# Kernel optimization log

Hardware: AMD Instinct MI355X
Metric: run time of the kernel (lower is better)

Reference implementation:

```python
import jax, jax.numpy as jnp
import numpy as np

L = 16            # number_of_grid_levels
T = 524288        # max_hash_table_entries (2^19)
F = 2             # hash_table_feature_dim
MIN_RES = 16      # coarsest_resolution
MAX_RES = 2048    # finest_resolution
WIDTH = 64        # mlp_width
OUT = 3           # output_channels
N = 1048576       # number of 2D query points
PRIME_Y = np.uint32(2654435761)  # NGP spatial hash prime for dim 1 (dim 0 prime = 1)


def _resolutions():
    g = np.exp((np.log(MAX_RES) - np.log(MIN_RES)) / (L - 1))
    return np.floor(MIN_RES * g ** np.arange(L)).astype(np.float32)  # [L]


def setup_inputs() -> dict:
    key = jax.random.key(0)
    ks = jax.random.split(key, 6)
    x = jax.random.uniform(ks[0], (N, 2), dtype=jnp.float32)
    # NGP hash tables are initialized small uniform
    tables = jax.random.uniform(ks[1], (L, T, F), minval=-1e-4, maxval=1e-4, dtype=jnp.float32)
    def dense(k, fi, fo):
        return (jax.random.normal(k, (fi, fo), dtype=jnp.float32) / np.sqrt(fi).astype(np.float32))
    W0 = dense(ks[2], L * F, WIDTH)
    W1 = dense(ks[3], WIDTH, WIDTH)
    W2 = dense(ks[4], WIDTH, OUT)
    return dict(x=x, tables=tables,
                W0=W0, b0=jnp.zeros((WIDTH,), jnp.float32),
                W1=W1, b1=jnp.zeros((WIDTH,), jnp.float32),
                W2=W2, b2=jnp.zeros((OUT,), jnp.float32))


def _hash_encode(x, tables):
    # Multi-resolution hash grid encoding (Instant-NGP, spatial_dim=2).
    res = jnp.asarray(_resolutions())                  # [L]
    scaled = x[:, None, :] * res[None, :, None]        # [N, L, 2]
    floored = jnp.floor(scaled)
    frac = scaled - floored                            # [N, L, 2]
    corners = jnp.array([[0, 0], [1, 0], [0, 1], [1, 1]], dtype=jnp.int32)  # [4, 2]
    vert = floored.astype(jnp.int32)[:, :, None, :] + corners[None, None]   # [N, L, 4, 2]
    vu = vert.astype(jnp.uint32)
    h = vu[..., 0] ^ (vu[..., 1] * PRIME_Y)            # spatial hash (prime for dim0 is 1)
    idx = (h % jnp.uint32(T)).astype(jnp.int32)        # [N, L, 4]
    feats = tables[jnp.arange(L)[None, :, None], idx]  # [N, L, 4, F] gather per level
    # bilinear weights: prod over dims of frac (if corner==1) else 1-frac
    wd = jnp.where(corners[None, None] == 1, frac[:, :, None, :], 1.0 - frac[:, :, None, :])
    w = wd[..., 0] * wd[..., 1]                        # [N, L, 4]
    interp = jnp.einsum('nlc,nlcf->nlf', w, feats)     # [N, L, F]
    return interp.reshape(x.shape[0], L * F)           # [N, L*F]


def reference(x, tables, W0, b0, W1, b1, W2, b2):
    h = _hash_encode(x, tables)
    h = jax.nn.relu(h @ W0 + b0)
    h = jax.nn.relu(h @ W1 + b1)
    return jax.nn.sigmoid(h @ W2 + b2)   # [N, 3]
```

## Files before the change

### kernel.cpp

```cpp
#include <hip/hip_runtime.h>

#define LVLS  16
#define TSZ   524288u
#define TMASK (TSZ - 1u)
#define PRIME 2654435761u

__constant__ float RES[LVLS] = {16.f, 22.f, 30.f, 42.f, 58.f, 80.f, 111.f, 153.f,
                                212.f, 294.f, 406.f, 561.f, 776.f, 1072.f, 1482.f, 2048.f};

typedef __bf16 bf16x8 __attribute__((ext_vector_type(8)));
typedef float  f32x4  __attribute__((ext_vector_type(4)));

union Frag {
    uint4          q;
    unsigned       u[4];
    unsigned short s[8];
    bf16x8         v;
};

static __device__ __forceinline__ unsigned short f2bf(float f) {
    unsigned u = __float_as_uint(f);
    u += 0x7FFFu + ((u >> 16) & 1u);
    return (unsigned short)(u >> 16);
}
static __device__ __forceinline__ unsigned pack2(float a, float b) {
    return (unsigned)f2bf(a) | ((unsigned)f2bf(b) << 16);
}
static __device__ __forceinline__ void lds_fence() {
    asm volatile("s_waitcnt lgkmcnt(0)" ::: "memory");
}

static __device__ __forceinline__ unsigned encode_level(
    const float2 xy, const float res, const float* __restrict__ tbf)
{
    const float sx = xy.x * res, sy = xy.y * res;
    const float fx = floorf(sx),  fy = floorf(sy);
    const float ux = sx - fx,     uy = sy - fy;
    const unsigned ix = (unsigned)(int)fx, iy = (unsigned)(int)fy;
    const unsigned hy0 = iy * PRIME, hy1 = (iy + 1u) * PRIME;
    const unsigned i00 = (ix ^ hy0) & TMASK;
    const unsigned i01 = (ix ^ hy1) & TMASK;
    float2 f00, f10, f01, f11;
    if (!(ix & 1u)) {
        const f32x4 a = *(const f32x4*)(tbf + 2u * (i00 & ~1u));
        const f32x4 b = *(const f32x4*)(tbf + 2u * (i01 & ~1u));
        const bool s0 = (i00 & 1u) != 0u;
        const bool s1 = (i01 & 1u) != 0u;
        f00 = s0 ? make_float2(a[2], a[3]) : make_float2(a[0], a[1]);
        f10 = s0 ? make_float2(a[0], a[1]) : make_float2(a[2], a[3]);
        f01 = s1 ? make_float2(b[2], b[3]) : make_float2(b[0], b[1]);
        f11 = s1 ? make_float2(b[0], b[1]) : make_float2(b[2], b[3]);
    } else {
        const unsigned i10 = ((ix + 1u) ^ hy0) & TMASK;
        const unsigned i11 = ((ix + 1u) ^ hy1) & TMASK;
        const float2* tb2 = (const float2*)tbf;
        f00 = tb2[i00]; f10 = tb2[i10];
        f01 = tb2[i01]; f11 = tb2[i11];
    }
    const float w00 = (1.f - ux) * (1.f - uy);
    const float w10 = ux * (1.f - uy);
    const float w01 = (1.f - ux) * uy;
    const float w11 = ux * uy;
    const float e0 = w00*f00.x + w10*f10.x + w01*f01.x + w11*f11.x;
    const float e1 = w00*f00.y + w10*f10.y + w01*f01.y + w11*f11.y;
    return pack2(e0, e1);
}

#define DENSE_TOTAL 3628

__global__ __launch_bounds__(256) void ngp_dehash(
    const float* __restrict__ tables, float2* __restrict__ dense)
{
    const int e = blockIdx.x * 256 + (int)threadIdx.x;
    if (e >= DENSE_TOTAL) return;
    int l, base;
    if      (e >= 1779) { l = 3; base = 1779; }
    else if (e >=  818) { l = 2; base =  818; }
    else if (e >=  289) { l = 1; base =  289; }
    else                { l = 0; base =    0; }
    const int Wd = (l == 0) ? 17 : (l == 1) ? 23 : (l == 2) ? 31 : 43;
    const int r  = e - base;
    const unsigned iy = (unsigned)(r / Wd), ix = (unsigned)(r % Wd);
    const unsigned h = (ix ^ (iy * PRIME)) & TMASK;
    dense[e] = ((const float2*)(tables + (size_t)l * (TSZ * 2u)))[h];
}

__global__ __launch_bounds__(256) void ngp_encode_fine(
    const float* __restrict__ x, const float* __restrict__ tables,
    unsigned* __restrict__ feat, int N)
{
    const int g = blockIdx.x;
    const int r = g & 7;
    const int l = 8 + r;
    const int n = (g >> 3) * 256 + (int)threadIdx.x;
    if (n >= N) return;
    const float2 xy = ((const float2*)x)[n];
    const float* tbf = tables + (size_t)l * (TSZ * 2u);
    feat[(size_t)r * N + n] = encode_level(xy, RES[l], tbf);
}

#define CLVL 8
#define SFEAT_BYTES (8 * CLVL * 64 * 4)
#define SB0_BYTES   (4 * 64 * 16)
#define SB1_BYTES   (8 * 64 * 16)
#define SDENSE_BYTES (DENSE_TOTAL * 8)
#define REGION_BYTES (SB0_BYTES + SB1_BYTES + SDENSE_BYTES)

__global__ __launch_bounds__(512, 4) void ngp_fused(
    const float* __restrict__ x, const float* __restrict__ tables,
    const float2* __restrict__ dense_g,
    const unsigned* __restrict__ feat,
    const float* __restrict__ W0, const float* __restrict__ b0,
    const float* __restrict__ W1, const float* __restrict__ b1,
    const float* __restrict__ W2, const float* __restrict__ b2,
    float* __restrict__ out, int N)
{
    __shared__ __align__(16) unsigned char smem[SFEAT_BYTES + REGION_BYTES];
    unsigned* sfeat = (unsigned*)smem;
    uint4*    sB0   = (uint4*)(smem + SFEAT_BYTES);
    uint4*    sB1   = (uint4*)(smem + SFEAT_BYTES + SB0_BYTES);
    float2*   sdense = (float2*)(smem + SFEAT_BYTES + SB0_BYTES + SB1_BYTES);
    unsigned short (*hscr)[16][72] =
        (unsigned short (*)[16][72])(smem + SFEAT_BYTES);

    const int tid  = threadIdx.x;
    const int lane = tid & 63;
    const int w    = tid >> 6;
    const int c    = lane & 15;
    const int quad = lane >> 4;

    {
        const int f = w;
        if (f < 4) {
            Frag t0;
            #pragma unroll
            for (int j = 0; j < 8; ++j)
                t0.s[j] = f2bf(W0[(quad * 8 + j) * 64 + f * 16 + c]);
            sB0[f * 64 + lane] = t0.q;
        }
        {
            const int kt = f >> 2, tt = f & 3;
            Frag t1;
            #pragma unroll
            for (int j = 0; j < 8; ++j)
                t1.s[j] = f2bf(W1[(kt * 32 + quad * 8 + j) * 64 + tt * 16 + c]);
            sB1[f * 64 + lane] = t1.q;
        }
        for (int e = tid; e < DENSE_TOTAL; e += 512)
            sdense[e] = dense_g[e];
    }
    __syncthreads();

    const int n = blockIdx.x * 512 + tid;
    if (n < N) {
        const float2 xy = ((const float2*)x)[n];
        #pragma unroll
        for (int l = 0; l < 4; ++l) {
            const int off = (l == 0) ? 0 : (l == 1) ? 289 : (l == 2) ? 818 : 1779;
            const int Wd  = (l == 0) ? 17 : (l == 1) ? 23 : (l == 2) ? 31 : 43;
            const float res = RES[l];
            const float sx = xy.x * res, sy = xy.y * res;
            const float fx = floorf(sx),  fy = floorf(sy);
            const float ux = sx - fx,     uy = sy - fy;
            const int ix = (int)fx, iy = (int)fy;
            const int b = off + iy * Wd + ix;
            const float2 f00 = sdense[b],      f10 = sdense[b + 1];
            const float2 f01 = sdense[b + Wd], f11 = sdense[b + Wd + 1];
            const float w00 = (1.f - ux) * (1.f - uy);
            const float w10 = ux * (1.f - uy);
            const float w01 = (1.f - ux) * uy;
            const float w11 = ux * uy;
            const float e0 = w00*f00.x + w10*f10.x + w01*f01.x + w11*f11.x;
            const float e1 = w00*f00.y + w10*f10.y + w01*f01.y + w11*f11.y;
            sfeat[(w * CLVL + l) * 64 + (lane ^ (((l >> 2) & 1) << 4))] = pack2(e0, e1);
        }
        #pragma unroll 2
        for (int l = 4; l < CLVL; ++l) {
            const float* tbf = tables + (size_t)l * (TSZ * 2u);
            const unsigned p = encode_level(xy, RES[l], tbf);
            sfeat[(w * CLVL + l) * 64 + (lane ^ (((l >> 2) & 1) << 4))] = p;
        }
    }
    __syncthreads();

    Frag B0f[4], B1f[8], B2f[2];
    #pragma unroll
    for (int t = 0; t < 4; ++t) B0f[t].q = sB0[t * 64 + lane];
    #pragma unroll
    for (int f = 0; f < 8; ++f) B1f[f].q = sB1[f * 64 + lane];
    #pragma unroll
    for (int f = 0; f < 2; ++f) {
        #pragma unroll
        for (int j = 0; j < 8; ++j) {
            const float v = (c < 3) ? W2[(f * 32 + quad * 8 + j) * 3 + c] : 0.f;
            B2f[f].s[j] = f2bf(v);
        }
    }

    float bias0[4], bias1[4];
    #pragma unroll
    for (int t = 0; t < 4; ++t) { bias0[t] = b0[t * 16 + c]; bias1[t] = b1[t * 16 + c]; }
    const float bias2 = (c < 3) ? b2[c] : 0.f;

    __syncthreads();

    #pragma unroll 1
    for (int it = 0; it < 4; ++it) {
        const int n0 = blockIdx.x * 512 + w * 64 + it * 16;

        Frag a0;
        if (quad < 2) {
            #pragma unroll
            for (int i = 0; i < 4; ++i)
                a0.u[i] = sfeat[(w * CLVL + quad * 4 + i) * 64 + ((it * 16 + c) ^ (quad << 4))];
        } else {
            #pragma unroll
            for (int i = 0; i < 4; ++i)
                a0.u[i] = feat[(size_t)((quad - 2) * 4 + i) * N + n0 + c];
        }

        f32x4 acc0[4];
        #pragma unroll
        for (int t = 0; t < 4; ++t) {
            f32x4 cin = {bias0[t], bias0[t], bias0[t], bias0[t]};
            acc0[t] = __builtin_amdgcn_mfma_f32_16x16x32_bf16(a0.v, B0f[t].v, cin, 0, 0, 0);
        }

        lds_fence();
        #pragma unroll
        for (int t = 0; t < 4; ++t)
            #pragma unroll
            for (int rr = 0; rr < 4; ++rr)
                hscr[w][quad * 4 + rr][t * 16 + c] = f2bf(fmaxf(acc0[t][rr], 0.f));

        lds_fence();
        Frag a1[2];
        #pragma unroll
        for (int kt = 0; kt < 2; ++kt)
            a1[kt].q = *(const uint4*)&hscr[w][c][kt * 32 + quad * 8];

        f32x4 acc1[4];
        #pragma unroll
        for (int t = 0; t < 4; ++t) {
            f32x4 cin = {bias1[t], bias1[t], bias1[t], bias1[t]};
            cin = __builtin_amdgcn_mfma_f32_16x16x32_bf16(a1[0].v, B1f[t].v, cin, 0, 0, 0);
            acc1[t] = __builtin_amdgcn_mfma_f32_16x16x32_bf16(a1[1].v, B1f[4 + t].v, cin, 0, 0, 0);
        }

        lds_fence();
        #pragma unroll
        for (int t = 0; t < 4; ++t)
            #pragma unroll
            for (int rr = 0; rr < 4; ++rr)
                hscr[w][quad * 4 + rr][t * 16 + c] = f2bf(fmaxf(acc1[t][rr], 0.f));

        lds_fence();
        Frag a2[2];
        #pragma unroll
        for (int kt = 0; kt < 2; ++kt)
            a2[kt].q = *(const uint4*)&hscr[w][c][kt * 32 + quad * 8];

        f32x4 cin2 = {bias2, bias2, bias2, bias2};
        cin2 = __builtin_amdgcn_mfma_f32_16x16x32_bf16(a2[0].v, B2f[0].v, cin2, 0, 0, 0);
        f32x4 acc2 = __builtin_amdgcn_mfma_f32_16x16x32_bf16(a2[1].v, B2f[1].v, cin2, 0, 0, 0);

        if (c < 3) {
            #pragma unroll
            for (int rr = 0; rr < 4; ++rr) {
                if (n0 + quad * 4 + rr < N) {
                    const float s = 1.f / (1.f + __expf(-acc2[rr]));
                    out[(size_t)(n0 + quad * 4 + rr) * 3 + c] = s;
                }
            }
        }
    }
}

extern "C" void kernel_launch(void* const* d_in, const int* in_sizes, int n_in,
                              void* d_out, int out_size, void* d_ws, size_t ws_size,
                              hipStream_t stream) {
    const float* x      = (const float*)d_in[0];
    const float* tables = (const float*)d_in[1];
    const float* W0     = (const float*)d_in[2];
    const float* b0     = (const float*)d_in[3];
    const float* W1     = (const float*)d_in[4];
    const float* b1     = (const float*)d_in[5];
    const float* W2     = (const float*)d_in[6];
    const float* b2     = (const float*)d_in[7];
    float* out = (float*)d_out;
    (void)ws_size; (void)n_in; (void)out_size;

    const int N  = in_sizes[0] / 2;
    unsigned* feat  = (unsigned*)d_ws;
    float2*   dense = (float2*)((char*)d_ws + (size_t)8 * N * 4);

    const int FB = (N + 255) / 256;
    const int PB = (N + 511) / 512;
    ngp_dehash<<<(DENSE_TOTAL + 255) / 256, 256, 0, stream>>>(tables, dense);
    ngp_encode_fine<<<8 * FB, 256, 0, stream>>>(x, tables, feat, N);
    ngp_fused<<<PB, 512, 0, stream>>>(x, tables, dense, feat,
                                      W0, b0, W1, b1, W2, b2, out, N);
}
```

Before: 260.5 us.

## Precompute dense corner-pair tables for mid levels and process two points per fine-encode thread

Adds a kernel that de-hashes levels 4-7 into dense tables where each entry holds the x-adjacent corner pair. The fused kernel then needs two 16-byte loads per level instead of four scattered hash-table gathers. The fine-level encoder now handles two points per thread to raise memory-level parallelism. The cost is an extra small launch and about 0.7 MB of workspace.

```diff
diff --git a/kernel.cpp b/kernel.cpp
--- a/kernel.cpp
+++ b/kernel.cpp
@@ -7,6 +7,10 @@
 
 __constant__ float RES[LVLS] = {16.f, 22.f, 30.f, 42.f, 58.f, 80.f, 111.f, 153.f,
                                 212.f, 294.f, 406.f, 561.f, 776.f, 1072.f, 1482.f, 2048.f};
+
+__constant__ int PRES[4] = {58, 80, 111, 153};
+__constant__ int POFF[4] = {0, 3422, 9902, 22334};
+#define PAIR_TOTAL 45896
 
 typedef __bf16 bf16x8 __attribute__((ext_vector_type(8)));
 typedef float  f32x4  __attribute__((ext_vector_type(4)));
@@ -85,6 +89,23 @@
     dense[e] = ((const float2*)(tables + (size_t)l * (TSZ * 2u)))[h];
 }
 
+__global__ __launch_bounds__(256) void ngp_dehash_pair(
+    const float* __restrict__ tables, f32x4* __restrict__ pairs)
+{
+    const int li = blockIdx.y;
+    const int res = PRES[li];
+    const int cnt = (res + 1) * res;
+    const int e = blockIdx.x * 256 + (int)threadIdx.x;
+    if (e >= cnt) return;
+    const unsigned iy = (unsigned)(e / res), ix = (unsigned)(e % res);
+    const unsigned hy = iy * PRIME;
+    const float2* tb2 = (const float2*)(tables + (size_t)(4 + li) * (TSZ * 2u));
+    const float2 v0 = tb2[(ix ^ hy) & TMASK];
+    const float2 v1 = tb2[((ix + 1u) ^ hy) & TMASK];
+    f32x4 p; p[0] = v0.x; p[1] = v0.y; p[2] = v1.x; p[3] = v1.y;
+    pairs[POFF[li] + e] = p;
+}
+
 __global__ __launch_bounds__(256) void ngp_encode_fine(
     const float* __restrict__ x, const float* __restrict__ tables,
     unsigned* __restrict__ feat, int N)
@@ -92,11 +113,18 @@
     const int g = blockIdx.x;
     const int r = g & 7;
     const int l = 8 + r;
-    const int n = (g >> 3) * 256 + (int)threadIdx.x;
-    if (n >= N) return;
-    const float2 xy = ((const float2*)x)[n];
+    const int n0 = (g >> 3) * 512 + (int)threadIdx.x;
+    const int n1 = n0 + 256;
     const float* tbf = tables + (size_t)l * (TSZ * 2u);
-    feat[(size_t)r * N + n] = encode_level(xy, RES[l], tbf);
+    const float res = RES[l];
+    float2 xy0, xy1;
+    if (n0 < N) xy0 = ((const float2*)x)[n0];
+    if (n1 < N) xy1 = ((const float2*)x)[n1];
+    unsigned p0 = 0, p1 = 0;
+    if (n0 < N) p0 = encode_level(xy0, res, tbf);
+    if (n1 < N) p1 = encode_level(xy1, res, tbf);
+    if (n0 < N) feat[(size_t)r * N + n0] = p0;
+    if (n1 < N) feat[(size_t)r * N + n1] = p1;
 }
 
 #define CLVL 8
@@ -107,8 +135,9 @@
 #define REGION_BYTES (SB0_BYTES + SB1_BYTES + SDENSE_BYTES)
 
 __global__ __launch_bounds__(512, 4) void ngp_fused(
-    const float* __restrict__ x, const float* __restrict__ tables,
+    const float* __restrict__ x,
     const float2* __restrict__ dense_g,
+    const f32x4* __restrict__ pairs,
     const unsigned* __restrict__ feat,
     const float* __restrict__ W0, const float* __restrict__ b0,
     const float* __restrict__ W1, const float* __restrict__ b1,
@@ -174,11 +203,25 @@
             const float e1 = w00*f00.y + w10*f10.y + w01*f01.y + w11*f11.y;
             sfeat[(w * CLVL + l) * 64 + (lane ^ (((l >> 2) & 1) << 4))] = pack2(e0, e1);
         }
-        #pragma unroll 2
-        for (int l = 4; l < CLVL; ++l) {
-            const float* tbf = tables + (size_t)l * (TSZ * 2u);
-            const unsigned p = encode_level(xy, RES[l], tbf);
-            sfeat[(w * CLVL + l) * 64 + (lane ^ (((l >> 2) & 1) << 4))] = p;
+        #pragma unroll
+        for (int li = 0; li < 4; ++li) {
+            const int l = 4 + li;
+            const float res = RES[l];
+            const int Wp = PRES[li];
+            const float sx = xy.x * res, sy = xy.y * res;
+            const float fx = floorf(sx),  fy = floorf(sy);
+            const float ux = sx - fx,     uy = sy - fy;
+            const int ix = (int)fx, iy = (int)fy;
+            const int b = POFF[li] + iy * Wp + ix;
+            const f32x4 r0 = pairs[b];
+            const f32x4 r1 = pairs[b + Wp];
+            const float w00 = (1.f - ux) * (1.f - uy);
+            const float w10 = ux * (1.f - uy);
+            const float w01 = (1.f - ux) * uy;
+            const float w11 = ux * uy;
+            const float e0 = w00*r0[0] + w10*r0[2] + w01*r1[0] + w11*r1[2];
+            const float e1 = w00*r0[1] + w10*r0[3] + w01*r1[1] + w11*r1[3];
+            sfeat[(w * CLVL + l) * 64 + (lane ^ (((l >> 2) & 1) << 4))] = pack2(e0, e1);
         }
     }
     __syncthreads();
@@ -293,11 +336,16 @@
     const int N  = in_sizes[0] / 2;
     unsigned* feat  = (unsigned*)d_ws;
     float2*   dense = (float2*)((char*)d_ws + (size_t)8 * N * 4);
-
-    const int FB = (N + 255) / 256;
+    f32x4*    pairs = (f32x4*)((char*)d_ws + (size_t)8 * N * 4 + DENSE_TOTAL * 8);
+
+    const int FB = (N + 511) / 512;
     const int PB = (N + 511) / 512;
     ngp_dehash<<<(DENSE_TOTAL + 255) / 256, 256, 0, stream>>>(tables, dense);
+    {
+        dim3 g((153 * 154 + 255) / 256, 4);
+        ngp_dehash_pair<<<g, 256, 0, stream>>>(tables, pairs);
+    }
     ngp_encode_fine<<<8 * FB, 256, 0, stream>>>(x, tables, feat, N);
-    ngp_fused<<<PB, 512, 0, stream>>>(x, tables, dense, feat,
+    ngp_fused<<<PB, 512, 0, stream>>>(x, dense, pairs, feat,
                                       W0, b0, W1, b1, W2, b2, out, N);
 }
```

Result: no change. 264.7 us (+1.6%).
